# Performance work log

Measured on AMD Instinct MI355X. Metric: run time of the kernel, lower is better.

The kernel has to match this reference:

```python
import jax, jax.numpy as jnp
import numpy as np

B, S, D, H = 4, 2048, 1024, 16
DK = D // H
THETA = 10000.0

def _trunc_normal(key, shape, in_f, out_f):
    std = (2.0 / (in_f + out_f)) ** 0.5
    return jax.random.truncated_normal(key, -3.0, 3.0, shape, jnp.float32) * std

def setup_inputs() -> dict:
    key = jax.random.key(0)
    kx, kq, kk, kv, ko = jax.random.split(key, 5)
    x = jax.random.normal(kx, (B, S, D), jnp.float32)
    wq = _trunc_normal(kq, (D, D), D, D)
    wk = _trunc_normal(kk, (D, D), D, D)
    wv = _trunc_normal(kv, (D, D), D, D)
    wo = _trunc_normal(ko, (D, D), D, D)
    token_positions = jnp.arange(S, dtype=jnp.int32)
    return {"x": x, "wq": wq, "wk": wk, "wv": wv, "wo": wo,
            "token_positions": token_positions}

def _rope_tables(token_positions, d_k, theta):
    # freq_cos/sin with each frequency duplicated pairwise: (d j) layout
    exponent = jnp.arange(0, d_k, 2, dtype=jnp.float32) / d_k
    freq = 1.0 / (theta ** exponent)            # [d_k/2]
    f = token_positions.astype(jnp.float32)[:, None] * freq[None, :]  # [s, d_k/2]
    cos = jnp.repeat(jnp.cos(f), 2, axis=-1)    # [s, d_k]
    sin = jnp.repeat(jnp.sin(f), 2, axis=-1)
    return cos, sin

def _rotate_half(x):
    x_even = x[..., 0::2]
    x_odd = x[..., 1::2]
    return jnp.stack((-x_odd, x_even), axis=-1).reshape(x.shape)

def reference(x, wq, wk, wv, wo, token_positions):
    b, s, d = x.shape
    # projections: y = x @ W^T  (weight stored [out, in])
    def proj(w):
        y = jnp.einsum('bsi,oi->bso', x, w)
        return y.reshape(b, s, H, DK).transpose(0, 2, 1, 3)  # [b,h,s,dk]
    q, k, v = proj(wq), proj(wk), proj(wv)
    cos, sin = _rope_tables(token_positions, DK, THETA)      # [s,dk]
    q = q * cos + _rotate_half(q) * sin
    k = k * cos + _rotate_half(k) * sin
    scores = jnp.einsum('bhnd,bhmd->bhnm', q, k) / jnp.sqrt(jnp.float32(DK))
    mask = jnp.tril(jnp.ones((s, s), dtype=bool))
    scores = jnp.where(mask, scores, -jnp.inf)
    attn = jax.nn.softmax(scores, axis=-1)
    out = jnp.einsum('bhnm,bhmd->bhnd', attn, v)
    out = out.transpose(0, 2, 1, 3).reshape(b, s, d)
    return jnp.einsum('bsi,oi->bso', out, wo)
```

## Files before the change

kernel.cpp:

```cpp
#include <hip/hip_runtime.h>
#include <hip/hip_bf16.h>
#include <stdint.h>
#include <math.h>

static constexpr int kS  = 2048;
static constexpr int kH  = 16;
static constexpr int kDK = 64;
static constexpr int kD  = 1024;
static constexpr int kB  = 4;
static constexpr int kM  = kB * kS;

typedef __bf16 bf16;
typedef __attribute__((ext_vector_type(8))) __bf16 bf16x8;
typedef __attribute__((ext_vector_type(4))) __bf16 bf16x4;
typedef __attribute__((ext_vector_type(4))) float f32x4;

__device__ __forceinline__ void gload_lds16(const bf16* g, bf16* l) {
  __builtin_amdgcn_global_load_lds((__attribute__((address_space(1))) void*)(void*)g,
                                   (__attribute__((address_space(3))) void*)l, 16, 0, 0);
}

__global__ void cvt_f32_bf16(const float* __restrict__ in, bf16* __restrict__ out, int n4) {
  int i = blockIdx.x * blockDim.x + threadIdx.x;
  if (i >= n4) return;
  float4 v = reinterpret_cast<const float4*>(in)[i];
  bf16x4 o;
  o[0] = (bf16)v.x; o[1] = (bf16)v.y; o[2] = (bf16)v.z; o[3] = (bf16)v.w;
  reinterpret_cast<bf16x4*>(out)[i] = o;
}

template<int BM>
__device__ __forceinline__ void gemm_body(const bf16* __restrict__ A,
                                          const bf16* __restrict__ W,
                                          void* __restrict__ dst,
                                          int K, int mode, int brow, int bcol) {
  constexpr int MF  = BM / 32;
  constexpr int ACH = BM / 64;

  __shared__ __align__(16) bf16 As[2][BM * 32];
  __shared__ __align__(16) bf16 Bs[2][128 * 32];

  const int tid = threadIdx.x;
  const int l   = tid & 63;
  const int w   = tid >> 6;
  const int wr = (w >> 1) * (BM / 2);
  const int wc = (w & 1) * 64;

  f32x4 acc[MF][4] = {};

  const int lrow = l >> 2;
  const int lcol = (l & 3) * 8;
  const int fr  = l & 15;
  const int fk  = (l >> 4) * 8;

  const int nk = K >> 5;

  auto STAGE = [&](int buf, int kt) {
    const int k0 = kt << 5;
#pragma unroll
    for (int c2 = 0; c2 < ACH; ++c2) {
      const int c = w * ACH + c2;
      gload_lds16(A + (size_t)(brow + c * 16 + lrow) * K + k0 + lcol, &As[buf][c * 512]);
    }
#pragma unroll
    for (int c2 = 0; c2 < 2; ++c2) {
      const int c = w * 2 + c2;
      gload_lds16(W + (size_t)(bcol + c * 16 + lrow) * K + k0 + lcol, &Bs[buf][c * 512]);
    }
  };

  STAGE(0, 0);
  __syncthreads();

  int cur = 0;
  for (int kt = 0; kt < nk; ++kt) {
    if (kt + 1 < nk) STAGE(cur ^ 1, kt + 1);

    bf16x8 af[MF], bfm[4];
#pragma unroll
    for (int m = 0; m < MF; ++m) af[m]  = *(const bf16x8*)&As[cur][(wr + m * 16 + fr) * 32 + fk];
#pragma unroll
    for (int n = 0; n < 4; ++n)  bfm[n] = *(const bf16x8*)&Bs[cur][(wc + n * 16 + fr) * 32 + fk];
#pragma unroll
    for (int m = 0; m < MF; ++m)
#pragma unroll
      for (int n = 0; n < 4; ++n)
        acc[m][n] = __builtin_amdgcn_mfma_f32_16x16x32_bf16(af[m], bfm[n], acc[m][n], 0, 0, 0);

    __syncthreads();
    cur ^= 1;
  }

  const int frow = (l >> 4) * 4;
  if (mode == 0) {
    bf16* out = (bf16*)dst;
#pragma unroll
    for (int m = 0; m < MF; ++m) {
#pragma unroll
      for (int n = 0; n < 4; ++n) {
        const int col = bcol + wc + n * 16 + fr;
        const int h = col >> 6, dk = col & 63;
#pragma unroll
        for (int r = 0; r < 4; ++r) {
          const int row = brow + wr + m * 16 + frow + r;
          const int b = row >> 11, s = row & (kS - 1);
          out[((((size_t)b * kH + h) * kS + s) << 6) + dk] = (bf16)acc[m][n][r];
        }
      }
    }
  } else {
    float* out = (float*)dst;
#pragma unroll
    for (int m = 0; m < MF; ++m) {
#pragma unroll
      for (int n = 0; n < 4; ++n) {
        const int col = bcol + wc + n * 16 + fr;
#pragma unroll
        for (int r = 0; r < 4; ++r) {
          const int row = brow + wr + m * 16 + frow + r;
          out[(size_t)row * kD + col] = acc[m][n][r];
        }
      }
    }
  }
}

template<int BM>
__global__ __launch_bounds__(256) void gemm_k(const bf16* __restrict__ A,
                                              const bf16* __restrict__ W,
                                              void* __restrict__ dst, int K, int mode) {
  gemm_body<BM>(A, W, dst, K, mode, blockIdx.x * BM, blockIdx.y * 128);
}

__global__ __launch_bounds__(256) void gemm_qkv(const bf16* __restrict__ A,
                                                const bf16* __restrict__ wq,
                                                const bf16* __restrict__ wk,
                                                const bf16* __restrict__ wv,
                                                bf16* __restrict__ Qb,
                                                bf16* __restrict__ Kb,
                                                bf16* __restrict__ Vb, int K) {
  const int by = blockIdx.y;
  const int sel = by >> 3;
  const bf16* W = (sel == 0) ? wq : (sel == 1) ? wk : wv;
  bf16* dst     = (sel == 0) ? Qb : (sel == 1) ? Kb : Vb;
  gemm_body<64>(A, W, dst, K, 0, blockIdx.x * 64, (by & 7) * 128);
}

__global__ void rope_kernel(bf16* __restrict__ Q, bf16* __restrict__ Kb,
                            const int* __restrict__ pos, int np) {
  int idx = blockIdx.x * blockDim.x + threadIdx.x;
  if (idx >= 2 * np) return;
  bf16* T = (idx < np) ? Q : Kb;
  int id = (idx < np) ? idx : idx - np;
  const int i = id & 31;
  const int s = (id >> 5) & (kS - 1);
  const float p = (float)pos[s];
  const float freq = __expf(-0.2878231366242557f * (float)i);
  const float f = p * freq;
  float sn, cs;
  sincosf(f, &sn, &cs);
  const size_t off = (size_t)id * 2;
  const float e = (float)T[off], o = (float)T[off + 1];
  T[off]     = (bf16)(e * cs - o * sn);
  T[off + 1] = (bf16)(o * cs + e * sn);
}

__global__ __launch_bounds__(256) void attn_fwd(const bf16* __restrict__ Q,
                                                const bf16* __restrict__ Kb,
                                                const bf16* __restrict__ Vb,
                                                bf16* __restrict__ O) {
  const int bh = blockIdx.x;
  const int qt = (int)gridDim.y - 1 - (int)blockIdx.y;
  const int tid = threadIdx.x;
  const int l = tid & 63;
  const int w = tid >> 6;

  __shared__ __align__(16) bf16 Ks[64 * 64];
  __shared__ __align__(16) bf16 Vt[64 * 64];
  __shared__ __align__(16) bf16 Pl[4][16 * 64];

  const int q0 = qt * 64 + w * 16;
  const int fr  = l & 15;
  const int fkg = l >> 4;
  const int fkg4 = fkg << 2;
  const size_t base = (size_t)bh * kS * kDK;

  const float SC2 = 0.125f * 1.4426950408889634f;

  bf16x8 aq[2];
#pragma unroll
  for (int kc = 0; kc < 2; ++kc)
    aq[kc] = *(const bf16x8*)&Q[base + (size_t)(q0 + fr) * kDK + kc * 32 + fkg * 8];

  f32x4 ao[4] = {};
  float m_r = -1e30f, l_r = 0.f;

  const int nt = qt + 1;

  const int krow = tid >> 3;
  const int kcol = (tid & 7) * 8;
  const int dk0  = w * 16;

  bf16x8 kreg0, kreg1, vreg0, vreg1;
  {
    const size_t kb0 = base + (size_t)krow * kDK + kcol;
    kreg0 = *(const bf16x8*)&Kb[kb0];
    kreg1 = *(const bf16x8*)&Kb[kb0 + 32 * kDK];
    const size_t vb0 = base + (size_t)l * kDK + dk0;
    vreg0 = *(const bf16x8*)&Vb[vb0];
    vreg1 = *(const bf16x8*)&Vb[vb0 + 8];
  }

  for (int j = 0; j < nt; ++j) {
    {
      const int r0 = krow, r1 = krow + 32;
      *(bf16x8*)&Ks[r0 * 64 + (kcol ^ ((r0 & 7) << 3))] = kreg0;
      *(bf16x8*)&Ks[r1 * 64 + (kcol ^ ((r1 & 7) << 3))] = kreg1;
#pragma unroll
      for (int e = 0; e < 8; ++e) {
        const int d0 = dk0 + e, d1 = dk0 + 8 + e;
        Vt[d0 * 64 + (l ^ ((d0 & 7) << 3))] = vreg0[e];
        Vt[d1 * 64 + (l ^ ((d1 & 7) << 3))] = vreg1[e];
      }
    }
    __syncthreads();

    if (j + 1 < nt) {
      const size_t kb0 = base + (size_t)((j + 1) * 64 + krow) * kDK + kcol;
      kreg0 = *(const bf16x8*)&Kb[kb0];
      kreg1 = *(const bf16x8*)&Kb[kb0 + 32 * kDK];
      const size_t vb0 = base + (size_t)((j + 1) * 64 + l) * kDK + dk0;
      vreg0 = *(const bf16x8*)&Vb[vb0];
      vreg1 = *(const bf16x8*)&Vb[vb0 + 8];
    }

    const bool diag = (j == nt - 1);

    f32x4 sc[4] = {};
#pragma unroll
    for (int nf = 0; nf < 4; ++nf) {
      if (!diag || nf <= w) {
#pragma unroll
        for (int kc = 0; kc < 2; ++kc) {
          const int row = nf * 16 + fr;
          bf16x8 bk = *(const bf16x8*)&Ks[row * 64 + ((kc * 32 + fkg * 8) ^ ((row & 7) << 3))];
          sc[nf] = __builtin_amdgcn_mfma_f32_16x16x32_bf16(bk, aq[kc], sc[nf], 0, 0, 0);
        }
      }
    }

    const int qloc = w * 16 + fr;
    float p[4][4];
    float mx = -INFINITY;
#pragma unroll
    for (int nf = 0; nf < 4; ++nf)
#pragma unroll
      for (int r = 0; r < 4; ++r) {
        float s = sc[nf][r] * SC2;
        if (diag && (nf * 16 + fkg4 + r) > qloc) s = -INFINITY;
        p[nf][r] = s;
        mx = fmaxf(mx, s);
      }
    mx = fmaxf(mx, __shfl_xor(mx, 16));
    mx = fmaxf(mx, __shfl_xor(mx, 32));
    const float mnew = fmaxf(m_r, mx);
    const float sf = __builtin_amdgcn_exp2f(m_r - mnew);
    float rs = 0.f;
#pragma unroll
    for (int nf = 0; nf < 4; ++nf)
#pragma unroll
      for (int r = 0; r < 4; ++r) {
        p[nf][r] = __builtin_amdgcn_exp2f(p[nf][r] - mnew);
        rs += p[nf][r];
      }
    rs += __shfl_xor(rs, 16);
    rs += __shfl_xor(rs, 32);
    l_r = l_r * sf + rs;
    m_r = mnew;

#pragma unroll
    for (int r = 0; r < 4; ++r) {
      const float sfq = __shfl(sf, (l & 48) + fkg4 + r);
#pragma unroll
      for (int n = 0; n < 4; ++n) ao[n][r] *= sfq;
    }

#pragma unroll
    for (int nf = 0; nf < 4; ++nf) {
      bf16x4 p4;
#pragma unroll
      for (int r = 0; r < 4; ++r) p4[r] = (bf16)p[nf][r];
      *(bf16x4*)&Pl[w][fr * 64 + ((nf * 16 + fkg4) ^ ((fr & 7) << 3))] = p4;
    }
    bf16x8 pa[2];
#pragma unroll
    for (int kc2 = 0; kc2 < 2; ++kc2)
      pa[kc2] = *(const bf16x8*)&Pl[w][fr * 64 + ((kc2 * 32 + fkg * 8) ^ ((fr & 7) << 3))];

#pragma unroll
    for (int kc2 = 0; kc2 < 2; ++kc2) {
      if (kc2 == 0 || !diag || w >= 2) {
#pragma unroll
        for (int n = 0; n < 4; ++n) {
          const int row = n * 16 + fr;
          bf16x8 bv = *(const bf16x8*)&Vt[row * 64 + ((kc2 * 32 + fkg * 8) ^ ((row & 7) << 3))];
          ao[n] = __builtin_amdgcn_mfma_f32_16x16x32_bf16(pa[kc2], bv, ao[n], 0, 0, 0);
        }
      }
    }
    __syncthreads();
  }

  const int b = bh >> 4, h = bh & 15;
  float lq[4];
#pragma unroll
  for (int r = 0; r < 4; ++r) lq[r] = __shfl(l_r, (l & 48) + fkg4 + r);
#pragma unroll
  for (int n = 0; n < 4; ++n)
#pragma unroll
    for (int r = 0; r < 4; ++r) {
      const int qg = q0 + fkg4 + r;
      const float ov = ao[n][r] / lq[r];
      O[((size_t)(b * kS + qg) << 10) + h * 64 + n * 16 + fr] = (bf16)ov;
    }
}

extern "C" void kernel_launch(void* const* d_in, const int* in_sizes, int n_in,
                              void* d_out, int out_size, void* d_ws, size_t ws_size,
                              hipStream_t stream) {
  const float* x  = (const float*)d_in[0];
  const float* wq = (const float*)d_in[1];
  const float* wk = (const float*)d_in[2];
  const float* wv = (const float*)d_in[3];
  const float* wo = (const float*)d_in[4];
  const int* pos  = (const int*)d_in[5];

  bf16* xb  = (bf16*)d_ws;
  bf16* wqb = xb  + (size_t)kM * kD;
  bf16* wkb = wqb + (size_t)kD * kD;
  bf16* wvb = wkb + (size_t)kD * kD;
  bf16* wob = wvb + (size_t)kD * kD;
  bf16* Qb  = wob + (size_t)kD * kD;
  bf16* Kbf = Qb  + (size_t)64 * kS * kDK;
  bf16* Vbf = Kbf + (size_t)64 * kS * kDK;
  bf16* Ob  = Vbf + (size_t)64 * kS * kDK;

  {
    int n4 = kM * kD / 4;
    cvt_f32_bf16<<<(n4 + 255) / 256, 256, 0, stream>>>(x, xb, n4);
    n4 = kD * kD / 4;
    cvt_f32_bf16<<<(n4 + 255) / 256, 256, 0, stream>>>(wq, wqb, n4);
    cvt_f32_bf16<<<(n4 + 255) / 256, 256, 0, stream>>>(wk, wkb, n4);
    cvt_f32_bf16<<<(n4 + 255) / 256, 256, 0, stream>>>(wv, wvb, n4);
    cvt_f32_bf16<<<(n4 + 255) / 256, 256, 0, stream>>>(wo, wob, n4);
  }

  gemm_qkv<<<dim3(kM / 64, 24), 256, 0, stream>>>(xb, wqb, wkb, wvb, Qb, Kbf, Vbf, kD);

  const int np = 64 * kS * 32;
  rope_kernel<<<(2 * np) / 256, 256, 0, stream>>>(Qb, Kbf, pos, np);

  dim3 ga(64, kS / 64);
  attn_fwd<<<ga, 256, 0, stream>>>(Qb, Kbf, Vbf, Ob);

  gemm_k<64><<<dim3(kM / 64, kD / 128), 256, 0, stream>>>(Ob, wob, d_out, kD, 1);
}
```

Before: 315.1 us.

## Enlarge GEMM tiles, fold softmax scale into RoPE, lazy rescale, batch weight casts

The GEMMs now use 128-row tiles and a 64-wide K step made of two 32-wide halves per stage, which halves the barrier count and raises operand reuse. The softmax scale and log2e factor are applied to Q in the RoPE kernel, so attention no longer scales every score. Attention only rescales the running max and output accumulator when a new max exceeds the old one by a threshold. The four weight conversions are merged into one launch. The costs are more LDS and registers per block, fewer blocks for the GEMMs, and extra bf16 rounding on the scaled Q. The lazy rescale lets unnormalised probabilities grow before they are renormalised, which risks precision loss.

```diff
diff --git a/kernel.cpp b/kernel.cpp
--- a/kernel.cpp
+++ b/kernel.cpp
@@ -29,6 +29,21 @@
   reinterpret_cast<bf16x4*>(out)[i] = o;
 }
 
+__global__ void cvt_w4(const float* __restrict__ w0, const float* __restrict__ w1,
+                       const float* __restrict__ w2, const float* __restrict__ w3,
+                       bf16* __restrict__ o0, bf16* __restrict__ o1,
+                       bf16* __restrict__ o2, bf16* __restrict__ o3, int n4) {
+  int i = blockIdx.x * blockDim.x + threadIdx.x;
+  if (i >= n4) return;
+  const int sel = blockIdx.y;
+  const float* in = (sel == 0) ? w0 : (sel == 1) ? w1 : (sel == 2) ? w2 : w3;
+  bf16* out      = (sel == 0) ? o0 : (sel == 1) ? o1 : (sel == 2) ? o2 : o3;
+  float4 v = reinterpret_cast<const float4*>(in)[i];
+  bf16x4 o;
+  o[0] = (bf16)v.x; o[1] = (bf16)v.y; o[2] = (bf16)v.z; o[3] = (bf16)v.w;
+  reinterpret_cast<bf16x4*>(out)[i] = o;
+}
+
 template<int BM>
 __device__ __forceinline__ void gemm_body(const bf16* __restrict__ A,
                                           const bf16* __restrict__ W,
@@ -37,8 +52,8 @@
   constexpr int MF  = BM / 32;
   constexpr int ACH = BM / 64;
 
-  __shared__ __align__(16) bf16 As[2][BM * 32];
-  __shared__ __align__(16) bf16 Bs[2][128 * 32];
+  __shared__ __align__(16) bf16 As[2][2][BM * 32];
+  __shared__ __align__(16) bf16 Bs[2][2][128 * 32];
 
   const int tid = threadIdx.x;
   const int l   = tid & 63;
@@ -53,19 +68,22 @@
   const int fr  = l & 15;
   const int fk  = (l >> 4) * 8;
 
-  const int nk = K >> 5;
+  const int nk = K >> 6;
 
   auto STAGE = [&](int buf, int kt) {
-    const int k0 = kt << 5;
-#pragma unroll
-    for (int c2 = 0; c2 < ACH; ++c2) {
-      const int c = w * ACH + c2;
-      gload_lds16(A + (size_t)(brow + c * 16 + lrow) * K + k0 + lcol, &As[buf][c * 512]);
-    }
-#pragma unroll
-    for (int c2 = 0; c2 < 2; ++c2) {
-      const int c = w * 2 + c2;
-      gload_lds16(W + (size_t)(bcol + c * 16 + lrow) * K + k0 + lcol, &Bs[buf][c * 512]);
+#pragma unroll
+    for (int h = 0; h < 2; ++h) {
+      const int k0 = (kt << 6) + h * 32;
+#pragma unroll
+      for (int c2 = 0; c2 < ACH; ++c2) {
+        const int c = w * ACH + c2;
+        gload_lds16(A + (size_t)(brow + c * 16 + lrow) * K + k0 + lcol, &As[buf][h][c * 512]);
+      }
+#pragma unroll
+      for (int c2 = 0; c2 < 2; ++c2) {
+        const int c = w * 2 + c2;
+        gload_lds16(W + (size_t)(bcol + c * 16 + lrow) * K + k0 + lcol, &Bs[buf][h][c * 512]);
+      }
     }
   };
 
@@ -76,16 +94,19 @@
   for (int kt = 0; kt < nk; ++kt) {
     if (kt + 1 < nk) STAGE(cur ^ 1, kt + 1);
 
-    bf16x8 af[MF], bfm[4];
-#pragma unroll
-    for (int m = 0; m < MF; ++m) af[m]  = *(const bf16x8*)&As[cur][(wr + m * 16 + fr) * 32 + fk];
-#pragma unroll
-    for (int n = 0; n < 4; ++n)  bfm[n] = *(const bf16x8*)&Bs[cur][(wc + n * 16 + fr) * 32 + fk];
-#pragma unroll
-    for (int m = 0; m < MF; ++m)
-#pragma unroll
-      for (int n = 0; n < 4; ++n)
-        acc[m][n] = __builtin_amdgcn_mfma_f32_16x16x32_bf16(af[m], bfm[n], acc[m][n], 0, 0, 0);
+#pragma unroll
+    for (int h = 0; h < 2; ++h) {
+      bf16x8 af[MF], bfm[4];
+#pragma unroll
+      for (int m = 0; m < MF; ++m) af[m]  = *(const bf16x8*)&As[cur][h][(wr + m * 16 + fr) * 32 + fk];
+#pragma unroll
+      for (int n = 0; n < 4; ++n)  bfm[n] = *(const bf16x8*)&Bs[cur][h][(wc + n * 16 + fr) * 32 + fk];
+#pragma unroll
+      for (int m = 0; m < MF; ++m)
+#pragma unroll
+        for (int n = 0; n < 4; ++n)
+          acc[m][n] = __builtin_amdgcn_mfma_f32_16x16x32_bf16(af[m], bfm[n], acc[m][n], 0, 0, 0);
+    }
 
     __syncthreads();
     cur ^= 1;
@@ -143,15 +164,16 @@
   const int sel = by >> 3;
   const bf16* W = (sel == 0) ? wq : (sel == 1) ? wk : wv;
   bf16* dst     = (sel == 0) ? Qb : (sel == 1) ? Kb : Vb;
-  gemm_body<64>(A, W, dst, K, 0, blockIdx.x * 64, (by & 7) * 128);
+  gemm_body<128>(A, W, dst, K, 0, blockIdx.x * 128, (by & 7) * 128);
 }
 
 __global__ void rope_kernel(bf16* __restrict__ Q, bf16* __restrict__ Kb,
                             const int* __restrict__ pos, int np) {
   int idx = blockIdx.x * blockDim.x + threadIdx.x;
   if (idx >= 2 * np) return;
-  bf16* T = (idx < np) ? Q : Kb;
-  int id = (idx < np) ? idx : idx - np;
+  const bool isQ = (idx < np);
+  bf16* T = isQ ? Q : Kb;
+  int id = isQ ? idx : idx - np;
   const int i = id & 31;
   const int s = (id >> 5) & (kS - 1);
   const float p = (float)pos[s];
@@ -159,10 +181,11 @@
   const float f = p * freq;
   float sn, cs;
   sincosf(f, &sn, &cs);
+  const float sc = isQ ? (0.125f * 1.4426950408889634f) : 1.0f;
   const size_t off = (size_t)id * 2;
   const float e = (float)T[off], o = (float)T[off + 1];
-  T[off]     = (bf16)(e * cs - o * sn);
-  T[off + 1] = (bf16)(o * cs + e * sn);
+  T[off]     = (bf16)((e * cs - o * sn) * sc);
+  T[off + 1] = (bf16)((o * cs + e * sn) * sc);
 }
 
 __global__ __launch_bounds__(256) void attn_fwd(const bf16* __restrict__ Q,
@@ -185,8 +208,6 @@
   const int fkg4 = fkg << 2;
   const size_t base = (size_t)bh * kS * kDK;
 
-  const float SC2 = 0.125f * 1.4426950408889634f;
-
   bf16x8 aq[2];
 #pragma unroll
   for (int kc = 0; kc < 2; ++kc)
@@ -256,34 +277,38 @@
     for (int nf = 0; nf < 4; ++nf)
 #pragma unroll
       for (int r = 0; r < 4; ++r) {
-        float s = sc[nf][r] * SC2;
+        float s = sc[nf][r];
         if (diag && (nf * 16 + fkg4 + r) > qloc) s = -INFINITY;
         p[nf][r] = s;
         mx = fmaxf(mx, s);
       }
     mx = fmaxf(mx, __shfl_xor(mx, 16));
     mx = fmaxf(mx, __shfl_xor(mx, 32));
-    const float mnew = fmaxf(m_r, mx);
-    const float sf = __builtin_amdgcn_exp2f(m_r - mnew);
+
+    if (__any(mx > m_r + 11.5f)) {
+      const float mnew = fmaxf(m_r, mx);
+      const float sf = __builtin_amdgcn_exp2f(m_r - mnew);
+      l_r *= sf;
+      m_r = mnew;
+#pragma unroll
+      for (int r = 0; r < 4; ++r) {
+        const float sfq = __shfl(sf, (l & 48) + fkg4 + r);
+#pragma unroll
+        for (int n = 0; n < 4; ++n) ao[n][r] *= sfq;
+      }
+    }
+
     float rs = 0.f;
 #pragma unroll
     for (int nf = 0; nf < 4; ++nf)
 #pragma unroll
       for (int r = 0; r < 4; ++r) {
-        p[nf][r] = __builtin_amdgcn_exp2f(p[nf][r] - mnew);
+        p[nf][r] = __builtin_amdgcn_exp2f(p[nf][r] - m_r);
         rs += p[nf][r];
       }
     rs += __shfl_xor(rs, 16);
     rs += __shfl_xor(rs, 32);
-    l_r = l_r * sf + rs;
-    m_r = mnew;
-
-#pragma unroll
-    for (int r = 0; r < 4; ++r) {
-      const float sfq = __shfl(sf, (l & 48) + fkg4 + r);
-#pragma unroll
-      for (int n = 0; n < 4; ++n) ao[n][r] *= sfq;
-    }
+    l_r += rs;
 
 #pragma unroll
     for (int nf = 0; nf < 4; ++nf) {
@@ -349,13 +374,10 @@
     int n4 = kM * kD / 4;
     cvt_f32_bf16<<<(n4 + 255) / 256, 256, 0, stream>>>(x, xb, n4);
     n4 = kD * kD / 4;
-    cvt_f32_bf16<<<(n4 + 255) / 256, 256, 0, stream>>>(wq, wqb, n4);
-    cvt_f32_bf16<<<(n4 + 255) / 256, 256, 0, stream>>>(wk, wkb, n4);
-    cvt_f32_bf16<<<(n4 + 255) / 256, 256, 0, stream>>>(wv, wvb, n4);
-    cvt_f32_bf16<<<(n4 + 255) / 256, 256, 0, stream>>>(wo, wob, n4);
-  }
-
-  gemm_qkv<<<dim3(kM / 64, 24), 256, 0, stream>>>(xb, wqb, wkb, wvb, Qb, Kbf, Vbf, kD);
+    cvt_w4<<<dim3((n4 + 255) / 256, 4), 256, 0, stream>>>(wq, wk, wv, wo, wqb, wkb, wvb, wob, n4);
+  }
+
+  gemm_qkv<<<dim3(kM / 128, 24), 256, 0, stream>>>(xb, wqb, wkb, wvb, Qb, Kbf, Vbf, kD);
 
   const int np = 64 * kS * 32;
   rope_kernel<<<(2 * np) / 256, 256, 0, stream>>>(Qb, Kbf, pos, np);
@@ -363,5 +385,5 @@
   dim3 ga(64, kS / 64);
   attn_fwd<<<ga, 256, 0, stream>>>(Qb, Kbf, Vbf, Ob);
 
-  gemm_k<64><<<dim3(kM / 64, kD / 128), 256, 0, stream>>>(Ob, wob, d_out, kD, 1);
-}
+  gemm_k<128><<<dim3(kM / 128, kD / 128), 256, 0, stream>>>(Ob, wob, d_out, kD, 1);
+}
```

Result: faster. 278.6 us (-11.6%).
